# Performance work log

Measured on AMD Instinct MI355X. Metric: run time of the kernel, lower is better.

## Reference

```python
import jax, jax.numpy as jnp
import numpy as np

HEIGHT = 32
WIDTH = 32
N = HEIGHT * WIDTH  # 1024 tokens
HEADS = 8
DIM_HEAD = 64
SCALE = DIM_HEAD ** -0.5


def _relative_pos_index_dis(h=HEIGHT, w=WIDTH):
    ch = np.arange(h)
    cw = np.arange(w)
    coords = np.stack(np.meshgrid(ch, cw, indexing='ij'))  # [2,h,w]
    flat = coords.reshape(2, -1)                            # [2,N]
    rel = flat[:, :, None] - flat[:, None, :]               # [2,N,N]
    rel = rel.transpose(1, 2, 0).astype(np.int64)           # [N,N,2]
    dis = (rel[:, :, 0].astype(np.float32) / h) ** 2 + (rel[:, :, 1].astype(np.float32) / w) ** 2
    rel[:, :, 0] += h - 1
    rel[:, :, 1] += w - 1
    rel[:, :, 0] *= 2 * w - 1
    idx = rel.sum(-1)
    return idx, dis

_REL_IDX_NP, _DIS_NP = _relative_pos_index_dis()
REL_IDX = jnp.asarray(_REL_IDX_NP)   # [N,N] int
DIS = jnp.asarray(_DIS_NP)           # [N,N] float32


def setup_inputs() -> dict:
    key = jax.random.key(0)
    k1, k2, k3, k4, k5 = jax.random.split(key, 5)
    dim = 512
    inner = HEADS * DIM_HEAD
    x = jax.random.normal(k1, (8, N, dim), dtype=jnp.float32)
    W_qkv = jax.random.normal(k2, (dim, 3 * inner), dtype=jnp.float32) * (dim ** -0.5)
    W_out = jax.random.normal(k3, (inner, dim), dtype=jnp.float32) * (inner ** -0.5)
    b_out = jnp.zeros((dim,), dtype=jnp.float32)
    rel_bias_table = jax.random.normal(k4, ((2 * HEIGHT - 1) * (2 * WIDTH - 1), HEADS), dtype=jnp.float32) * 0.02
    # torch init: zeros + range(1,heads)*0.1 -> [0.1, 0.2, ..., 0.8]
    headsita = (jnp.arange(1, HEADS + 1, dtype=jnp.float32) * 0.1)
    return {"x": x, "W_qkv": W_qkv, "W_out": W_out, "b_out": b_out,
            "rel_bias_table": rel_bias_table, "headsita": headsita, "rpe": 1}


def reference(x, W_qkv, W_out, b_out, rel_bias_table, headsita, rpe):
    B = x.shape[0]
    qkv = x @ W_qkv                              # [B,N,3*inner]
    q, k, v = jnp.split(qkv, 3, axis=-1)
    def to_heads(t):
        return t.reshape(B, N, HEADS, DIM_HEAD).transpose(0, 2, 1, 3)  # [B,H,N,D]
    q, k, v = to_heads(q), to_heads(k), to_heads(v)
    dots0 = jnp.einsum('bhid,bhjd->bhij', q, k) * SCALE  # [B,H,N,N]
    if rpe:
        # gathered relative-position bias: [N,N,H] -> [H,N,N]
        rel_bias = rel_bias_table[REL_IDX].transpose(2, 0, 1)
        factor = 1.0 / (2.0 * headsita ** 2 + 1e-10)     # [H]
        pos_embed = jnp.exp(-factor[:, None, None] * DIS[None, :, :])  # [H,N,N]
        dots = dots0 + rel_bias[None] + 0.01 * pos_embed[None]
    else:
        dots = dots0
    attn = jax.nn.softmax(dots, axis=-1)
    out = jnp.einsum('bhij,bhjd->bhid', attn, v)          # [B,H,N,D]
    out = out.transpose(0, 2, 1, 3).reshape(B, N, HEADS * DIM_HEAD)
    out = out @ W_out + b_out
    return out, jax.nn.softmax(dots0, axis=-1)
```

## Files before the change

kernel.cpp:

```cpp
#include <hip/hip_runtime.h>
#include <hip/hip_bf16.h>

typedef __attribute__((ext_vector_type(8))) short bf16x8;
typedef __attribute__((ext_vector_type(4))) float f32x4;
typedef float f32x4u __attribute__((ext_vector_type(4), aligned(4)));
typedef __attribute__((ext_vector_type(4))) unsigned int uint32x4;

#define N_TOK 1024
#define HEADS 8
#define DIM_HEAD 64
#define BATCH 8
#define DIMM 512
#define INNER 512
#define QKV_COLS 1536

#define MFMA16 __builtin_amdgcn_mfma_f32_16x16x32_bf16

__device__ inline short f2bf(float f) {
  union { float f; unsigned u; } v;
  v.f = f;
  unsigned r = v.u + 0x7fffu + ((v.u >> 16) & 1u);
  return (short)(r >> 16);
}

__device__ inline unsigned pack2bf(float a, float b) {
  return ((unsigned)(unsigned short)f2bf(a)) | (((unsigned)(unsigned short)f2bf(b)) << 16);
}

__device__ inline void lds_barrier() {
  asm volatile("s_waitcnt lgkmcnt(0)" ::: "memory");
  __builtin_amdgcn_s_barrier();
  asm volatile("" ::: "memory");
}

__device__ inline void gload_lds16(const short* g, short* l) {
  __builtin_amdgcn_global_load_lds(
      (const __attribute__((address_space(1))) void*)g,
      (__attribute__((address_space(3))) void*)l, 16, 0, 0);
}

__global__ void cvt_bf16_kernel(const float* __restrict__ in, short* __restrict__ out, int n) {
  int i = (blockIdx.x * 256 + threadIdx.x) * 4;
  if (i >= n) return;
  float4 v = *(const float4*)&in[i];
  short4 o;
  o.x = f2bf(v.x); o.y = f2bf(v.y); o.z = f2bf(v.z); o.w = f2bf(v.w);
  *(short4*)&out[i] = o;
}

__global__ void tr_cvt_kernel(const float* __restrict__ W, short* __restrict__ Wt, int K, int Nc) {
  int id = blockIdx.x * 256 + threadIdx.x;
  if (id >= K * Nc) return;
  int n = id % Nc, k = id / Nc;
  Wt[n * K + k] = f2bf(W[id]);
}

__global__ void bias2e_kernel(const float* __restrict__ rel, const float* __restrict__ headsita,
                              float* __restrict__ bias2e) {
  int e = blockIdx.x * 256 + threadIdx.x;
  if (e >= HEADS * 4096) return;
  int h = e >> 12, idx = e & 4095;
  if (idx >= 3969) return;
  int dr = idx / 63 - 31;
  int dc = idx % 63 - 31;
  float th = headsita[h];
  float factor = 1.f / (2.f * th * th + 1e-10f);
  float dis = (float)(dr * dr + dc * dc) * (1.0f / 1024.0f);
  bias2e[e] = __expf(rel[idx * HEADS + h] + 0.01f * __expf(-factor * dis));
}

__global__ __launch_bounds__(256)
void kv_pack_kernel(const short* __restrict__ qkv, short* __restrict__ Kfrag,
                    short* __restrict__ Vfrag) {
  __shared__ short T[128][72];
  const int t = threadIdx.x;
  const int tile = blockIdx.x;
  const int bh = blockIdx.y;
  const int b = bh >> 3, h = bh & 7;
  if (tile < 16) {
    #pragma unroll
    for (int c = 0; c < 2; ++c) {
      int idn = c * 256 + t, j = idn >> 3, dc = (idn & 7) * 8;
      *(int4*)&T[j][dc] =
        *(const int4*)&qkv[(size_t)(b * N_TOK + tile * 64 + j) * QKV_COLS + INNER + h * DIM_HEAD + dc];
    }
    lds_barrier();
    #pragma unroll
    for (int c = 0; c < 2; ++c) {
      int fi = c * 256 + t, cidx = fi >> 6, l = fi & 63;
      int wv = cidx >> 1, f = cidx & 1;
      int4 v = *(const int4*)&T[wv * 16 + (l & 15)][f * 32 + (l >> 4) * 8];
      *(int4*)&Kfrag[(((size_t)bh * 16 + tile) * 8 + cidx) * 512 + l * 8] = v;
    }
  } else {
    const int w = tile - 16;
    #pragma unroll
    for (int c = 0; c < 4; ++c) {
      int idn = c * 256 + t, j = idn >> 3, dc = (idn & 7) * 8;
      *(int4*)&T[j][dc] =
        *(const int4*)&qkv[(size_t)(b * N_TOK + w * 128 + j) * QKV_COLS + 2 * INNER + h * DIM_HEAD + dc];
    }
    lds_barrier();
    #pragma unroll
    for (int c = 0; c < 4; ++c) {
      int fi = c * 256 + t, cidx = fi >> 6, l = fi & 63;
      int wv = cidx >> 2, dt = cidx & 3;
      int rg = l >> 4, cl = l & 15;
      int jj = (rg >> 1) * 64 + wv * 16 + (rg & 1) * 8;
      int d = dt * 16 + cl;
      short tmp[8];
      #pragma unroll
      for (int e = 0; e < 8; ++e) tmp[e] = T[jj + e][d];
      *(int4*)&Vfrag[(((size_t)bh * 8 + w) * 16 + cidx) * 512 + l * 8] = *(int4*)tmp;
    }
  }
}

template<int OUT_BF16, int ADD_BIAS>
__global__ __launch_bounds__(256)
void gemm_kernel(const short* __restrict__ A, const short* __restrict__ Bt,
                 void* __restrict__ C, const float* __restrict__ bias,
                 int M, int Nc, int K, int lda)
{
  __shared__ short Ash[128 * 32];
  __shared__ short Bsh[128 * 32];
  const int t = threadIdx.x;
  const int lane = t & 63, wave = t >> 6;
  const int wm = wave >> 1, wn = wave & 1;
  const int m0 = blockIdx.y * 128, n0 = blockIdx.x * 128;
  const int grow = wave * 32 + (lane >> 2);
  const int gcol = (lane & 3) * 8;
  f32x4 acc[4][4] = {};
  for (int k0 = 0; k0 < K; k0 += 32) {
    lds_barrier();
    #pragma unroll
    for (int i = 0; i < 2; ++i) {
      gload_lds16(&A[(size_t)(m0 + grow + i * 16) * lda + k0 + gcol],
                  &Ash[(wave * 32 + i * 16) * 32]);
      gload_lds16(&Bt[(size_t)(n0 + grow + i * 16) * K + k0 + gcol],
                  &Bsh[(wave * 32 + i * 16) * 32]);
    }
    asm volatile("s_waitcnt vmcnt(0)" ::: "memory");
    __builtin_amdgcn_s_barrier();
    asm volatile("" ::: "memory");
    bf16x8 af[4], bfr[4];
    #pragma unroll
    for (int m = 0; m < 4; ++m)
      af[m] = *(const bf16x8*)&Ash[(wm * 64 + m * 16 + (lane & 15)) * 32 + (lane >> 4) * 8];
    #pragma unroll
    for (int n = 0; n < 4; ++n)
      bfr[n] = *(const bf16x8*)&Bsh[(wn * 64 + n * 16 + (lane & 15)) * 32 + (lane >> 4) * 8];
    #pragma unroll
    for (int m = 0; m < 4; ++m)
      #pragma unroll
      for (int n = 0; n < 4; ++n)
        acc[m][n] = MFMA16(af[m], bfr[n], acc[m][n], 0, 0, 0);
  }
  const int r0 = (lane >> 4) * 4, c0 = lane & 15;
  #pragma unroll
  for (int m = 0; m < 4; ++m)
    #pragma unroll
    for (int n = 0; n < 4; ++n) {
      int col = n0 + wn*64 + n*16 + c0;
      float bv = ADD_BIAS ? bias[col] : 0.f;
      #pragma unroll
      for (int r = 0; r < 4; ++r) {
        int row = m0 + wm*64 + m*16 + r0 + r;
        float v = acc[m][n][r] + bv;
        if (OUT_BF16) ((short*)C)[(size_t)row * Nc + col] = f2bf(v);
        else          ((float*)C)[(size_t)row * Nc + col] = v;
      }
    }
}

__global__ __launch_bounds__(256, 4)
void attn_kernel(short* qkv,
                 const short* __restrict__ Kfrag,
                 const short* __restrict__ Vfrag,
                 const float* __restrict__ bias2e,
                 const int* __restrict__ rpe_p,
                 float* __restrict__ out2)
{
  __shared__ __align__(16) char arena[17408];
  __shared__ float red0[4][16];
  __shared__ float red1[4][16];

  const int t = threadIdx.x;
  const int lane = t & 63, wv = t >> 6;
  const int rg = lane >> 4, cl = lane & 15;

  const int id = blockIdx.x;
  const int bh = (id & 7) * 8 + ((id >> 3) & 7);
  const int i0 = (id >> 6) * 16;
  const int b = bh >> 3, h = bh & 7;
  const size_t rowbase = (size_t)b * N_TOK;

  const size_t qoff = (rowbase + i0 + cl) * QKV_COLS + h * DIM_HEAD;
  const bf16x8 qf0 = *(const bf16x8*)&qkv[qoff + rg * 8];
  const bf16x8 qf1 = *(const bf16x8*)&qkv[qoff + 32 + rg * 8];

  const short* kf = Kfrag + (((size_t)bh * 16) * 8 + wv * 2) * 512 + lane * 8;
  f32x4 sc[16];
  bf16x8 a0 = *(const bf16x8*)&kf[0];
  bf16x8 a1 = *(const bf16x8*)&kf[512];
  #pragma unroll
  for (int tj = 0; tj < 16; ++tj) {
    bf16x8 n0, n1;
    if (tj < 15) {
      n0 = *(const bf16x8*)&kf[(tj + 1) * 4096];
      n1 = *(const bf16x8*)&kf[(tj + 1) * 4096 + 512];
    }
    f32x4 z = (f32x4){0.f, 0.f, 0.f, 0.f};
    z = MFMA16(a0, qf0, z, 0, 0, 0);
    z = MFMA16(a1, qf1, z, 0, 0, 0);
    sc[tj] = z;
    a0 = n0; a1 = n1;
  }

  float m = -1e30f;
  #pragma unroll
  for (int tj = 0; tj < 16; ++tj)
    #pragma unroll
    for (int r = 0; r < 4; ++r) m = fmaxf(m, sc[tj][r]);
  m = fmaxf(m, __shfl_xor(m, 16));
  m = fmaxf(m, __shfl_xor(m, 32));
  if (lane < 16) red0[wv][lane] = m;
  lds_barrier();
  m = fmaxf(fmaxf(red0[0][cl], red0[1][cl]), fmaxf(red0[2][cl], red0[3][cl]));

  float s = 0.f;
  #pragma unroll
  for (int tj = 0; tj < 16; ++tj)
    #pragma unroll
    for (int r = 0; r < 4; ++r) {
      float e = __expf((sc[tj][r] - m) * 0.125f);
      sc[tj][r] = e;
      s += e;
    }
  s += __shfl_xor(s, 16);
  s += __shfl_xor(s, 32);
  if (lane < 16) red1[wv][lane] = s;
  lds_barrier();
  const float sm0 = red1[0][cl] + red1[1][cl] + red1[2][cl] + red1[3][cl];
  const float iv0 = 1.f / sm0;

  float* stage = (float*)arena;
  const size_t o2base = ((size_t)(b * HEADS + h) * N_TOK + i0) * N_TOK;
  #pragma unroll
  for (int c = 0; c < 4; ++c) {
    #pragma unroll
    for (int tjl = 0; tjl < 4; ++tjl)
      #pragma unroll
      for (int r = 0; r < 4; ++r)
        stage[(tjl * 64 + wv * 16 + rg * 4 + r) * 17 + cl] = sc[c * 4 + tjl][r] * iv0;
    lds_barrier();
    #pragma unroll
    for (int k = 0; k < 4; ++k) {
      int row = wv * 4 + k;
      #pragma unroll
      for (int e = 0; e < 4; ++e) {
        float v = stage[(e * 64 + lane) * 17 + row];
        out2[o2base + (size_t)row * N_TOK + c * 256 + e * 64 + lane] = v;
      }
    }
    lds_barrier();
  }

  const int i_row = i0 + cl;
  const int ri = i_row >> 5, ci = i_row & 31;
  float iv1;
  if (rpe_p[0]) {
    const float* bt = bias2e + (h << 12);
    const int C = (ri - (wv >> 1)) * 63 + ci - ((wv & 1) * 16 + rg * 4) + 1984;
    float s1 = 0.f;
    #pragma unroll
    for (int tj = 0; tj < 16; ++tj) {
      f32x4u bv = *(const f32x4u*)&bt[C - tj * 126 - 3];
      float v0 = sc[tj][0] * bv[3];
      float v1 = sc[tj][1] * bv[2];
      float v2 = sc[tj][2] * bv[1];
      float v3 = sc[tj][3] * bv[0];
      sc[tj][0] = v0; sc[tj][1] = v1; sc[tj][2] = v2; sc[tj][3] = v3;
      s1 += (v0 + v1) + (v2 + v3);
    }
    s1 += __shfl_xor(s1, 16);
    s1 += __shfl_xor(s1, 32);
    if (lane < 16) red0[wv][lane] = s1;
    lds_barrier();
    iv1 = 1.f / (red0[0][cl] + red0[1][cl] + red0[2][cl] + red0[3][cl]);
  } else {
    iv1 = iv0;
  }

  unsigned short* P_c = (unsigned short*)arena;
  const short* vf = Vfrag + (((size_t)bh * 8) * 16 + wv * 4) * 512 + lane * 8;
  f32x4 oacc[4];
  #pragma unroll
  for (int dt = 0; dt < 4; ++dt) oacc[dt] = (f32x4){0.f, 0.f, 0.f, 0.f};
  #pragma unroll
  for (int ch = 0; ch < 2; ++ch) {
    #pragma unroll
    for (int tj8 = 0; tj8 < 8; ++tj8) {
      int tj = ch * 8 + tj8;
      unsigned u0 = pack2bf(sc[tj][0] * iv1, sc[tj][1] * iv1);
      unsigned u1 = pack2bf(sc[tj][2] * iv1, sc[tj][3] * iv1);
      uint2 uu; uu.x = u0; uu.y = u1;
      *(uint2*)&P_c[cl * 520 + wv * 130 + tj8 * 16 + rg * 4] = uu;
    }
    #pragma unroll
    for (int w4 = 0; w4 < 4; ++w4) {
      int w = ch * 4 + w4;
      int tjr = (2 * w + (rg >> 1)) & 7;
      bf16x8 pb = *(const bf16x8*)&P_c[cl * 520 + wv * 130 + tjr * 16 + (rg & 1) * 8];
      #pragma unroll
      for (int dt = 0; dt < 4; ++dt) {
        bf16x8 va = *(const bf16x8*)&vf[w * 8192 + dt * 512];
        oacc[dt] = MFMA16(va, pb, oacc[dt], 0, 0, 0);
      }
    }
  }

  lds_barrier();
  float* buf = (float*)arena;
  #pragma unroll
  for (int dt = 0; dt < 4; ++dt)
    #pragma unroll
    for (int r = 0; r < 4; ++r)
      buf[wv * 1040 + cl * 65 + dt * 16 + rg * 4 + r] = oacc[dt][r];
  lds_barrier();

  const int i_ = t >> 4, dq = t & 15;
  float o[4];
  #pragma unroll
  for (int k = 0; k < 4; ++k) {
    int d = dq * 4 + k;
    o[k] = buf[0 * 1040 + i_ * 65 + d] + buf[1 * 1040 + i_ * 65 + d]
         + buf[2 * 1040 + i_ * 65 + d] + buf[3 * 1040 + i_ * 65 + d];
  }
  short4 os;
  os.x = f2bf(o[0]); os.y = f2bf(o[1]); os.z = f2bf(o[2]); os.w = f2bf(o[3]);
  *(short4*)&qkv[(rowbase + i0 + i_) * QKV_COLS + h * DIM_HEAD + dq * 4] = os;
}

extern "C" void kernel_launch(void* const* d_in, const int* in_sizes, int n_in,
                              void* d_out, int out_size, void* d_ws, size_t ws_size,
                              hipStream_t stream) {
  const float* x    = (const float*)d_in[0];
  const float* Wqkv = (const float*)d_in[1];
  const float* Wout = (const float*)d_in[2];
  const float* bout = (const float*)d_in[3];
  const float* rel  = (const float*)d_in[4];
  const float* sita = (const float*)d_in[5];
  const int*   rpe  = (const int*)d_in[6];

  char* ws = (char*)d_ws;
  short* xb     = (short*)(ws);
  short* WqT    = (short*)(ws + 8388608);
  short* WoT    = (short*)(ws + 9961472);
  short* qkv    = (short*)(ws + 10485760);
  short* Kfrag  = (short*)(ws);
  short* Vfrag  = (short*)(ws + 35651584);
  float* bias2e = (float*)(ws + 8388608);

  float* out1 = (float*)d_out;
  float* out2 = out1 + (size_t)BATCH * N_TOK * DIMM;

  hipLaunchKernelGGL(cvt_bf16_kernel, dim3(4096), dim3(256), 0, stream,
                     x, xb, BATCH * N_TOK * DIMM);
  hipLaunchKernelGGL(tr_cvt_kernel, dim3((512 * 1536 + 255) / 256), dim3(256), 0, stream,
                     Wqkv, WqT, 512, 1536);
  hipLaunchKernelGGL(tr_cvt_kernel, dim3((512 * 512 + 255) / 256), dim3(256), 0, stream,
                     Wout, WoT, 512, 512);
  hipLaunchKernelGGL((gemm_kernel<1, 0>), dim3(12, 64), dim3(256), 0, stream,
                     xb, WqT, (void*)qkv, (const float*)nullptr, 8192, 1536, 512, 512);
  hipLaunchKernelGGL(bias2e_kernel, dim3((HEADS * 4096 + 255) / 256), dim3(256), 0, stream,
                     rel, sita, bias2e);
  hipLaunchKernelGGL(kv_pack_kernel, dim3(24, 64), dim3(256), 0, stream, qkv, Kfrag, Vfrag);
  hipLaunchKernelGGL(attn_kernel, dim3(4096), dim3(256), 0, stream,
                     qkv, Kfrag, Vfrag, bias2e, rpe, out2);
  hipLaunchKernelGGL((gemm_kernel<0, 1>), dim3(4, 64), dim3(256), 0, stream,
                     qkv, WoT, d_out, bout, 8192, 512, 512, 1536);
}
```

Measured before the change: 167.1 us.

## Fuse K/V fragment packing into QKV GEMM epilogue and merge prep kernels

```diff
diff --git a/kernel.cpp b/kernel.cpp
--- a/kernel.cpp
+++ b/kernel.cpp
@@ -39,87 +39,46 @@
       (__attribute__((address_space(3))) void*)l, 16, 0, 0);
 }
 
-__global__ void cvt_bf16_kernel(const float* __restrict__ in, short* __restrict__ out, int n) {
-  int i = (blockIdx.x * 256 + threadIdx.x) * 4;
-  if (i >= n) return;
-  float4 v = *(const float4*)&in[i];
-  short4 o;
-  o.x = f2bf(v.x); o.y = f2bf(v.y); o.z = f2bf(v.z); o.w = f2bf(v.w);
-  *(short4*)&out[i] = o;
-}
-
-__global__ void tr_cvt_kernel(const float* __restrict__ W, short* __restrict__ Wt, int K, int Nc) {
-  int id = blockIdx.x * 256 + threadIdx.x;
-  if (id >= K * Nc) return;
-  int n = id % Nc, k = id / Nc;
-  Wt[n * K + k] = f2bf(W[id]);
-}
-
-__global__ void bias2e_kernel(const float* __restrict__ rel, const float* __restrict__ headsita,
-                              float* __restrict__ bias2e) {
-  int e = blockIdx.x * 256 + threadIdx.x;
-  if (e >= HEADS * 4096) return;
-  int h = e >> 12, idx = e & 4095;
-  if (idx >= 3969) return;
-  int dr = idx / 63 - 31;
-  int dc = idx % 63 - 31;
-  float th = headsita[h];
-  float factor = 1.f / (2.f * th * th + 1e-10f);
-  float dis = (float)(dr * dr + dc * dc) * (1.0f / 1024.0f);
-  bias2e[e] = __expf(rel[idx * HEADS + h] + 0.01f * __expf(-factor * dis));
-}
-
 __global__ __launch_bounds__(256)
-void kv_pack_kernel(const short* __restrict__ qkv, short* __restrict__ Kfrag,
-                    short* __restrict__ Vfrag) {
-  __shared__ short T[128][72];
-  const int t = threadIdx.x;
-  const int tile = blockIdx.x;
-  const int bh = blockIdx.y;
-  const int b = bh >> 3, h = bh & 7;
-  if (tile < 16) {
-    #pragma unroll
-    for (int c = 0; c < 2; ++c) {
-      int idn = c * 256 + t, j = idn >> 3, dc = (idn & 7) * 8;
-      *(int4*)&T[j][dc] =
-        *(const int4*)&qkv[(size_t)(b * N_TOK + tile * 64 + j) * QKV_COLS + INNER + h * DIM_HEAD + dc];
-    }
-    lds_barrier();
-    #pragma unroll
-    for (int c = 0; c < 2; ++c) {
-      int fi = c * 256 + t, cidx = fi >> 6, l = fi & 63;
-      int wv = cidx >> 1, f = cidx & 1;
-      int4 v = *(const int4*)&T[wv * 16 + (l & 15)][f * 32 + (l >> 4) * 8];
-      *(int4*)&Kfrag[(((size_t)bh * 16 + tile) * 8 + cidx) * 512 + l * 8] = v;
-    }
+void prep_kernel(const float* __restrict__ x, short* __restrict__ xb,
+                 const float* __restrict__ Wqkv, short* __restrict__ WqT,
+                 const float* __restrict__ Wout, short* __restrict__ WoT,
+                 const float* __restrict__ rel, const float* __restrict__ headsita,
+                 float* __restrict__ bias2e) {
+  const int blk = blockIdx.x, t = threadIdx.x;
+  if (blk < 4096) {
+    int i = (blk * 256 + t) * 4;
+    float4 v = *(const float4*)&x[i];
+    short4 o;
+    o.x = f2bf(v.x); o.y = f2bf(v.y); o.z = f2bf(v.z); o.w = f2bf(v.w);
+    *(short4*)&xb[i] = o;
+  } else if (blk < 7168) {
+    int id = (blk - 4096) * 256 + t;
+    int n = id % 1536, k = id / 1536;
+    WqT[n * 512 + k] = f2bf(Wqkv[id]);
+  } else if (blk < 8192) {
+    int id = (blk - 7168) * 256 + t;
+    int n = id & 511, k = id >> 9;
+    WoT[n * 512 + k] = f2bf(Wout[id]);
   } else {
-    const int w = tile - 16;
-    #pragma unroll
-    for (int c = 0; c < 4; ++c) {
-      int idn = c * 256 + t, j = idn >> 3, dc = (idn & 7) * 8;
-      *(int4*)&T[j][dc] =
-        *(const int4*)&qkv[(size_t)(b * N_TOK + w * 128 + j) * QKV_COLS + 2 * INNER + h * DIM_HEAD + dc];
-    }
-    lds_barrier();
-    #pragma unroll
-    for (int c = 0; c < 4; ++c) {
-      int fi = c * 256 + t, cidx = fi >> 6, l = fi & 63;
-      int wv = cidx >> 2, dt = cidx & 3;
-      int rg = l >> 4, cl = l & 15;
-      int jj = (rg >> 1) * 64 + wv * 16 + (rg & 1) * 8;
-      int d = dt * 16 + cl;
-      short tmp[8];
-      #pragma unroll
-      for (int e = 0; e < 8; ++e) tmp[e] = T[jj + e][d];
-      *(int4*)&Vfrag[(((size_t)bh * 8 + w) * 16 + cidx) * 512 + l * 8] = *(int4*)tmp;
-    }
-  }
-}
-
-template<int OUT_BF16, int ADD_BIAS>
+    int e = (blk - 8192) * 256 + t;
+    int h = e >> 12, idx = e & 4095;
+    if (idx >= 3969) return;
+    int dr = idx / 63 - 31;
+    int dc = idx % 63 - 31;
+    float th = headsita[h];
+    float factor = 1.f / (2.f * th * th + 1e-10f);
+    float dis = (float)(dr * dr + dc * dc) * (1.0f / 1024.0f);
+    bias2e[e] = __expf(rel[idx * HEADS + h] + 0.01f * __expf(-factor * dis));
+  }
+}
+
+template<int SPLIT>
 __global__ __launch_bounds__(256)
 void gemm_kernel(const short* __restrict__ A, const short* __restrict__ Bt,
                  void* __restrict__ C, const float* __restrict__ bias,
+                 short* __restrict__ Qb, short* __restrict__ Kfrag,
+                 short* __restrict__ Vfrag,
                  int M, int Nc, int K, int lda)
 {
   __shared__ short Ash[128 * 32];
@@ -157,24 +116,59 @@
         acc[m][n] = MFMA16(af[m], bfr[n], acc[m][n], 0, 0, 0);
   }
   const int r0 = (lane >> 4) * 4, c0 = lane & 15;
-  #pragma unroll
-  for (int m = 0; m < 4; ++m)
-    #pragma unroll
-    for (int n = 0; n < 4; ++n) {
-      int col = n0 + wn*64 + n*16 + c0;
-      float bv = ADD_BIAS ? bias[col] : 0.f;
-      #pragma unroll
-      for (int r = 0; r < 4; ++r) {
-        int row = m0 + wm*64 + m*16 + r0 + r;
-        float v = acc[m][n][r] + bv;
-        if (OUT_BF16) ((short*)C)[(size_t)row * Nc + col] = f2bf(v);
-        else          ((float*)C)[(size_t)row * Nc + col] = v;
+  if (!SPLIT) {
+    #pragma unroll
+    for (int m = 0; m < 4; ++m)
+      #pragma unroll
+      for (int n = 0; n < 4; ++n) {
+        int col = n0 + wn*64 + n*16 + c0;
+        float bv = bias[col];
+        #pragma unroll
+        for (int r = 0; r < 4; ++r) {
+          int row = m0 + wm*64 + m*16 + r0 + r;
+          ((float*)C)[(size_t)row * Nc + col] = acc[m][n][r] + bv;
+        }
       }
-    }
+  } else {
+    const int seg = n0 >> 9;
+    #pragma unroll
+    for (int m = 0; m < 4; ++m)
+      #pragma unroll
+      for (int n = 0; n < 4; ++n) {
+        const int colg = n0 + wn*64 + n*16 + c0;
+        const int rowg0 = m0 + wm*64 + m*16 + r0;
+        if (seg == 0) {
+          #pragma unroll
+          for (int rr = 0; rr < 4; ++rr)
+            Qb[(size_t)(rowg0 + rr) * 512 + colg] = f2bf(acc[m][n][rr]);
+        } else if (seg == 1) {
+          const int d = colg - 512, h = d >> 6, dd = d & 63;
+          const int b = rowg0 >> 10, j0 = rowg0 & 1023;
+          const size_t base = ((((size_t)(b * 8 + h) * 16 + (j0 >> 6)) * 8)
+                               + ((j0 >> 4) & 3) * 2 + (dd >> 5)) * 512
+                              + ((dd >> 3) & 3) * 128 + (dd & 7);
+          #pragma unroll
+          for (int rr = 0; rr < 4; ++rr)
+            Kfrag[base + ((j0 + rr) & 15) * 8] = f2bf(acc[m][n][rr]);
+        } else {
+          const int d = colg - 1024, h = d >> 6, dd = d & 63;
+          const int b = rowg0 >> 10, j0 = rowg0 & 1023;
+          const int w = j0 >> 7, j7 = j0 & 127;
+          const int rgv = (((j7 >> 6) & 1) << 1) | ((j7 >> 3) & 1);
+          const int wvv = (j7 >> 4) & 3, e0 = j7 & 7;
+          const size_t addr = (((size_t)(b * 8 + h) * 8 + w) * 16 + wvv * 4 + (dd >> 4)) * 512
+                              + (rgv * 16 + (dd & 15)) * 8 + e0;
+          short4 sv;
+          sv.x = f2bf(acc[m][n][0]); sv.y = f2bf(acc[m][n][1]);
+          sv.z = f2bf(acc[m][n][2]); sv.w = f2bf(acc[m][n][3]);
+          *(short4*)&Vfrag[addr] = sv;
+        }
+      }
+  }
 }
 
 __global__ __launch_bounds__(256, 4)
-void attn_kernel(short* qkv,
+void attn_kernel(short* Qb,
                  const short* __restrict__ Kfrag,
                  const short* __restrict__ Vfrag,
                  const float* __restrict__ bias2e,
@@ -195,9 +189,9 @@
   const int b = bh >> 3, h = bh & 7;
   const size_t rowbase = (size_t)b * N_TOK;
 
-  const size_t qoff = (rowbase + i0 + cl) * QKV_COLS + h * DIM_HEAD;
-  const bf16x8 qf0 = *(const bf16x8*)&qkv[qoff + rg * 8];
-  const bf16x8 qf1 = *(const bf16x8*)&qkv[qoff + 32 + rg * 8];
+  const size_t qoff = (rowbase + i0 + cl) * 512 + h * DIM_HEAD;
+  const bf16x8 qf0 = *(const bf16x8*)&Qb[qoff + rg * 8];
+  const bf16x8 qf1 = *(const bf16x8*)&Qb[qoff + 32 + rg * 8];
 
   const short* kf = Kfrag + (((size_t)bh * 16) * 8 + wv * 2) * 512 + lane * 8;
   f32x4 sc[16];
@@ -339,7 +333,7 @@
   }
   short4 os;
   os.x = f2bf(o[0]); os.y = f2bf(o[1]); os.z = f2bf(o[2]); os.w = f2bf(o[3]);
-  *(short4*)&qkv[(rowbase + i0 + i_) * QKV_COLS + h * DIM_HEAD + dq * 4] = os;
+  *(short4*)&Qb[(rowbase + i0 + i_) * 512 + h * DIM_HEAD + dq * 4] = os;
 }
 
 extern "C" void kernel_launch(void* const* d_in, const int* in_sizes, int n_in,
@@ -357,27 +351,22 @@
   short* xb     = (short*)(ws);
   short* WqT    = (short*)(ws + 8388608);
   short* WoT    = (short*)(ws + 9961472);
-  short* qkv    = (short*)(ws + 10485760);
-  short* Kfrag  = (short*)(ws);
+  short* Qbuf   = (short*)(ws + 10485760);
+  short* Kfrag  = (short*)(ws + 18874368);
+  float* bias2e = (float*)(ws + 27262976);
   short* Vfrag  = (short*)(ws + 35651584);
-  float* bias2e = (float*)(ws + 8388608);
 
   float* out1 = (float*)d_out;
   float* out2 = out1 + (size_t)BATCH * N_TOK * DIMM;
 
-  hipLaunchKernelGGL(cvt_bf16_kernel, dim3(4096), dim3(256), 0, stream,
-                     x, xb, BATCH * N_TOK * DIMM);
-  hipLaunchKernelGGL(tr_cvt_kernel, dim3((512 * 1536 + 255) / 256), dim3(256), 0, stream,
-                     Wqkv, WqT, 512, 1536);
-  hipLaunchKernelGGL(tr_cvt_kernel, dim3((512 * 512 + 255) / 256), dim3(256), 0, stream,
-                     Wout, WoT, 512, 512);
-  hipLaunchKernelGGL((gemm_kernel<1, 0>), dim3(12, 64), dim3(256), 0, stream,
-                     xb, WqT, (void*)qkv, (const float*)nullptr, 8192, 1536, 512, 512);
-  hipLaunchKernelGGL(bias2e_kernel, dim3((HEADS * 4096 + 255) / 256), dim3(256), 0, stream,
-                     rel, sita, bias2e);
-  hipLaunchKernelGGL(kv_pack_kernel, dim3(24, 64), dim3(256), 0, stream, qkv, Kfrag, Vfrag);
+  hipLaunchKernelGGL(prep_kernel, dim3(8320), dim3(256), 0, stream,
+                     x, xb, Wqkv, WqT, Wout, WoT, rel, sita, bias2e);
+  hipLaunchKernelGGL((gemm_kernel<1>), dim3(12, 64), dim3(256), 0, stream,
+                     xb, WqT, (void*)nullptr, (const float*)nullptr,
+                     Qbuf, Kfrag, Vfrag, 8192, 1536, 512, 512);
   hipLaunchKernelGGL(attn_kernel, dim3(4096), dim3(256), 0, stream,
-                     qkv, Kfrag, Vfrag, bias2e, rpe, out2);
-  hipLaunchKernelGGL((gemm_kernel<0, 1>), dim3(4, 64), dim3(256), 0, stream,
-                     qkv, WoT, d_out, bout, 8192, 512, 512, 1536);
-}
+                     Qbuf, Kfrag, Vfrag, bias2e, rpe, out2);
+  hipLaunchKernelGGL((gemm_kernel<0>), dim3(4, 64), dim3(256), 0, stream,
+                     Qbuf, WoT, d_out, bout,
+                     (short*)nullptr, (short*)nullptr, (short*)nullptr, 8192, 512, 512, 512);
+}
```

After: 158.8 us. 5.0% less time.
